# Kernel optimization log

Measured on AMD Instinct MI355X. Metric: run time of the kernel, lower is better.

The kernel has to match this reference:

```python
import jax, jax.numpy as jnp
import numpy as np

N, D, H = 262144, 512, 128


def _mlp(x, W1, b1, W2, b2):
    # Linear -> ReLU -> Linear
    return jax.nn.relu(x @ W1 + b1) @ W2 + b2


def setup_inputs() -> dict:
    key = jax.random.key(0)
    ks = jax.random.split(key, 8)
    features = jax.random.normal(ks[0], (N, D), dtype=jnp.float32)
    # last column is the routing flag: 0 -> transform expert, nonzero -> actor expert
    flags = jax.random.randint(ks[1], (N,), 0, 2).astype(jnp.float32)
    features = features.at[:, -1].set(flags)
    s = 0.02
    return {
        "features": features,
        "Wt1": jax.random.normal(ks[2], (D, H), dtype=jnp.float32) * s,
        "bt1": jnp.zeros((H,), dtype=jnp.float32),
        "Wt2": jax.random.normal(ks[3], (H, H), dtype=jnp.float32) * s,
        "bt2": jnp.zeros((H,), dtype=jnp.float32),
        "Wa1": jax.random.normal(ks[4], (D, H), dtype=jnp.float32) * s,
        "ba1": jnp.zeros((H,), dtype=jnp.float32),
        "Wa2": jax.random.normal(ks[5], (H, H), dtype=jnp.float32) * s,
        "ba2": jnp.zeros((H,), dtype=jnp.float32),
        "Wv1": jax.random.normal(ks[6], (D, H), dtype=jnp.float32) * s,
        "bv1": jnp.zeros((H,), dtype=jnp.float32),
        "Wv2": jax.random.normal(ks[7], (H, H), dtype=jnp.float32) * s,
        "bv2": jnp.zeros((H,), dtype=jnp.float32),
    }


def reference(features, Wt1, bt1, Wt2, bt2, Wa1, ba1, Wa2, ba2, Wv1, bv1, Wv2, bv2):
    # forward_actor: per-row dispatch on flag = features[:, -1]
    # flag == 0 -> policy_transform_net, else -> policy_actor_net.
    # Equivalent vectorized form: compute both experts, select per row.
    flag_is_zero = (features[:, -1] == 0)[:, None]  # [N, 1]
    trans_out = _mlp(features, Wt1, bt1, Wt2, bt2)   # [N, H]
    actor_out = _mlp(features, Wa1, ba1, Wa2, ba2)   # [N, H]
    latent_pi = jnp.where(flag_is_zero, trans_out, actor_out)
    # forward_critic: Linear-ReLU-Linear-ReLU
    latent_vf = jax.nn.relu(_mlp(features, Wv1, bv1, Wv2, bv2))
    return latent_pi, latent_vf
```

## Files before the change

kernel.cpp:

```cpp
#include <hip/hip_runtime.h>

#define NTOK 262144L

typedef __attribute__((ext_vector_type(4))) float f32x4;
typedef __attribute__((ext_vector_type(8))) short bf16x8;

static __device__ __forceinline__ unsigned short f2bf(float f) {
  unsigned int u = __builtin_bit_cast(unsigned int, f);
  u += 0x7fffu + ((u >> 16) & 1u);
  return (unsigned short)(u >> 16);
}

__global__ void pack_w(const float* __restrict__ Wt1, const float* __restrict__ Wa1,
                       const float* __restrict__ Wv1, const float* __restrict__ Wt2,
                       const float* __restrict__ Wa2, const float* __restrict__ Wv2,
                       unsigned short* __restrict__ pk) {
  int idx = blockIdx.x * 256 + threadIdx.x;
  if (idx >= 245760) return;
  float v;
  if (idx < 196608) {
    int j = idx & 7, l = (idx >> 3) & 63, ct = (idx >> 9) & 7, kt = (idx >> 12) & 15, e = idx >> 16;
    const float* W = (e == 0) ? Wt1 : (e == 1) ? Wa1 : Wv1;
    v = W[(kt * 32 + ((l >> 4) * 8) + j) * 128 + ct * 16 + (l & 15)];
  } else {
    int i2 = idx - 196608;
    int j = i2 & 7, l = (i2 >> 3) & 63, ct = (i2 >> 9) & 7, kt = (i2 >> 12) & 3, e = i2 >> 14;
    const float* W = (e == 0) ? Wt2 : (e == 1) ? Wa2 : Wv2;
    v = W[(kt * 32 + ((l >> 4) * 8) + j) * 128 + ct * 16 + (l & 15)];
  }
  pk[idx] = f2bf(v);
}


__global__ __launch_bounds__(512, 4) void mlp3(
    const float* __restrict__ X, const unsigned short* __restrict__ pk,
    const float* __restrict__ bt1, const float* __restrict__ bt2,
    const float* __restrict__ ba1, const float* __restrict__ ba2,
    const float* __restrict__ bv1, const float* __restrict__ bv2,
    float* __restrict__ out) {
  __shared__ unsigned short Xs[2 * 64 * 128];
  __shared__ unsigned short Hs[3 * 64 * 128];
  const int t = threadIdx.x;
  const long brow = (long)blockIdx.x * 64;
  const int lane = t & 63;
  const int w = t >> 6;
  const int l15 = lane & 15;
  const int g = lane >> 4;

  const float4* __restrict__ Xv = (const float4*)(X + brow * 512);

  f32x4 at[4], aa[4], av[4];
  {
    float b0 = bt1[w * 16 + l15], b1v = ba1[w * 16 + l15], b2v = bv1[w * 16 + l15];
    #pragma unroll
    for (int rt = 0; rt < 4; ++rt) {
      at[rt] = (f32x4){b0, b0, b0, b0};
      aa[rt] = (f32x4){b1v, b1v, b1v, b1v};
      av[rt] = (f32x4){b2v, b2v, b2v, b2v};
    }
  }

  {
    float4 ld[4];
    #pragma unroll
    for (int i = 0; i < 4; ++i) {
      int f = t + 512 * i;
      ld[i] = Xv[(f >> 5) * 128 + (f & 31)];
    }
    #pragma unroll
    for (int i = 0; i < 4; ++i) {
      int f = t + 512 * i;
      int row = f >> 5, c4 = f & 31;
      unsigned long long p = (unsigned long long)f2bf(ld[i].x)
                           | ((unsigned long long)f2bf(ld[i].y) << 16)
                           | ((unsigned long long)f2bf(ld[i].z) << 32)
                           | ((unsigned long long)f2bf(ld[i].w) << 48);
      int addr = (row * 256 + c4 * 8) ^ ((row & 7) << 4);
      *(unsigned long long*)((char*)Xs + addr) = p;
    }
  }
  __syncthreads();

  unsigned fmask = 0;

  #pragma unroll
  for (int kc = 0; kc < 4; ++kc) {
    float4 nx[4];
    if (kc < 3) {
      #pragma unroll
      for (int i = 0; i < 4; ++i) {
        int f = t + 512 * i;
        nx[i] = Xv[(f >> 5) * 128 + (kc + 1) * 32 + (f & 31)];
      }
    }
    const char* xb = (const char*)Xs + (kc & 1) * 16384;
    #pragma unroll
    for (int ktl = 0; ktl < 4; ++ktl) {
      int kt = kc * 4 + ktl;
      int wo = ((kt * 8 + w) << 9) + (lane << 3);
      bf16x8 wt = *(const bf16x8*)(pk + wo);
      bf16x8 wa = *(const bf16x8*)(pk + 65536 + wo);
      bf16x8 wv = *(const bf16x8*)(pk + 131072 + wo);
      #pragma unroll
      for (int rt = 0; rt < 4; ++rt) {
        int row = rt * 16 + l15;
        bf16x8 a = *(const bf16x8*)(xb + ((row * 256 + ktl * 64 + g * 16) ^ ((row & 7) << 4)));
        at[rt] = __builtin_amdgcn_mfma_f32_16x16x32_bf16(a, wt, at[rt], 0, 0, 0);
        aa[rt] = __builtin_amdgcn_mfma_f32_16x16x32_bf16(a, wa, aa[rt], 0, 0, 0);
        av[rt] = __builtin_amdgcn_mfma_f32_16x16x32_bf16(a, wv, av[rt], 0, 0, 0);
      }
    }
    if (kc == 3) {
      #pragma unroll
      for (int rt = 0; rt < 4; ++rt)
        #pragma unroll
        for (int r = 0; r < 4; ++r) {
          int row = rt * 16 + 4 * g + r;
          unsigned short fv = *(const unsigned short*)((const char*)Xs + 16384 +
                               ((row * 256 + 254) ^ ((row & 7) << 4)));
          if (fv != 0) fmask |= 1u << (rt * 4 + r);
        }
    }
    if (kc < 3) {
      #pragma unroll
      for (int i = 0; i < 4; ++i) {
        int f = t + 512 * i;
        int row = f >> 5, c4 = f & 31;
        unsigned long long p = (unsigned long long)f2bf(nx[i].x)
                             | ((unsigned long long)f2bf(nx[i].y) << 16)
                             | ((unsigned long long)f2bf(nx[i].z) << 32)
                             | ((unsigned long long)f2bf(nx[i].w) << 48);
        int addr = ((kc + 1) & 1) * 16384 + ((row * 256 + c4 * 8) ^ ((row & 7) << 4));
        *(unsigned long long*)((char*)Xs + addr) = p;
      }
      __syncthreads();
    }
  }

  #pragma unroll
  for (int rt = 0; rt < 4; ++rt)
    #pragma unroll
    for (int r = 0; r < 4; ++r) {
      int row = rt * 16 + 4 * g + r;
      int col = w * 16 + l15;
      int ha = (row * 256 + col * 2) ^ ((row & 7) << 4) ^ ((row & 8) << 2);
      *(unsigned short*)((char*)Hs + ha)         = f2bf(fmaxf(at[rt][r], 0.f));
      *(unsigned short*)((char*)Hs + 16384 + ha) = f2bf(fmaxf(aa[rt][r], 0.f));
      *(unsigned short*)((char*)Hs + 32768 + ha) = f2bf(fmaxf(av[rt][r], 0.f));
    }
  __syncthreads();

  auto layer2 = [&](int e, const float* __restrict__ b2, f32x4 a2[4]) {
    float bv = b2[w * 16 + l15];
    #pragma unroll
    for (int rt = 0; rt < 4; ++rt) a2[rt] = (f32x4){bv, bv, bv, bv};
    const unsigned short* W2f = pk + 196608 + e * 16384;
    const char* hb = (const char*)Hs + e * 16384;
    #pragma unroll
    for (int kt = 0; kt < 4; ++kt) {
      bf16x8 wb = *(const bf16x8*)(W2f + ((kt * 8 + w) << 9) + (lane << 3));
      #pragma unroll
      for (int rt = 0; rt < 4; ++rt) {
        int row = rt * 16 + l15;
        bf16x8 a = *(const bf16x8*)(hb + ((row * 256 + kt * 64 + g * 16)
                      ^ ((row & 7) << 4) ^ ((row & 8) << 2)));
        a2[rt] = __builtin_amdgcn_mfma_f32_16x16x32_bf16(a, wb, a2[rt], 0, 0, 0);
      }
    }
  };

  f32x4 keep[4], a2[4];
  layer2(0, bt2, keep);
  layer2(1, ba2, a2);
  {
    const int col = w * 16 + l15;
    #pragma unroll
    for (int rt = 0; rt < 4; ++rt)
      #pragma unroll
      for (int r = 0; r < 4; ++r) {
        long row = brow + rt * 16 + 4 * g + r;
        float sel = ((fmask >> (rt * 4 + r)) & 1u) ? a2[rt][r] : keep[rt][r];
        out[row * 128 + col] = sel;
      }
  }
  layer2(2, bv2, a2);
  {
    const int col = w * 16 + l15;
    float* __restrict__ ov = out + NTOK * 128;
    #pragma unroll
    for (int rt = 0; rt < 4; ++rt)
      #pragma unroll
      for (int r = 0; r < 4; ++r) {
        long row = brow + rt * 16 + 4 * g + r;
        ov[row * 128 + col] = fmaxf(a2[rt][r], 0.f);
      }
  }
}

extern "C" void kernel_launch(void* const* d_in, const int* in_sizes, int n_in,
                              void* d_out, int out_size, void* d_ws, size_t ws_size,
                              hipStream_t stream) {
  const float* X   = (const float*)d_in[0];
  const float* Wt1 = (const float*)d_in[1];
  const float* bt1 = (const float*)d_in[2];
  const float* Wt2 = (const float*)d_in[3];
  const float* bt2 = (const float*)d_in[4];
  const float* Wa1 = (const float*)d_in[5];
  const float* ba1 = (const float*)d_in[6];
  const float* Wa2 = (const float*)d_in[7];
  const float* ba2 = (const float*)d_in[8];
  const float* Wv1 = (const float*)d_in[9];
  const float* bv1 = (const float*)d_in[10];
  const float* Wv2 = (const float*)d_in[11];
  const float* bv2 = (const float*)d_in[12];
  unsigned short* pk = (unsigned short*)d_ws;

  pack_w<<<960, 256, 0, stream>>>(Wt1, Wa1, Wv1, Wt2, Wa2, Wv2, pk);
  mlp3<<<4096, 512, 0, stream>>>(X, pk, bt1, bt2, ba1, ba2, bv1, bv2, (float*)d_out);
}
```

Baseline: 271.7 us.

## Halve row tile to 32 with 4 waves each covering two column tiles

Each block now handles 32 rows with 256 threads, and each wave computes two 16-column tiles instead of one, so every A fragment read from LDS feeds twice as many MFMAs. Layer-2 hidden buffers shrink from three to two by reusing H0 for the critic branch, which adds extra barriers. LDS per block drops substantially, aiming for more resident blocks and better latency hiding. In exchange, each block does twice as many weight loads per row processed, and the grid doubles.

```diff
diff --git a/kernel.cpp b/kernel.cpp
--- a/kernel.cpp
+++ b/kernel.cpp
@@ -32,16 +32,17 @@
 }
 
 
-__global__ __launch_bounds__(512, 4) void mlp3(
+__global__ __launch_bounds__(256, 4) void mlp3(
     const float* __restrict__ X, const unsigned short* __restrict__ pk,
     const float* __restrict__ bt1, const float* __restrict__ bt2,
     const float* __restrict__ ba1, const float* __restrict__ ba2,
     const float* __restrict__ bv1, const float* __restrict__ bv2,
     float* __restrict__ out) {
-  __shared__ unsigned short Xs[2 * 64 * 128];
-  __shared__ unsigned short Hs[3 * 64 * 128];
+  __shared__ unsigned short Xs[2 * 32 * 128];
+  __shared__ unsigned short H0[32 * 128];
+  __shared__ unsigned short H1[32 * 128];
   const int t = threadIdx.x;
-  const long brow = (long)blockIdx.x * 64;
+  const long brow = (long)blockIdx.x * 32;
   const int lane = t & 63;
   const int w = t >> 6;
   const int l15 = lane & 15;
@@ -49,14 +50,17 @@
 
   const float4* __restrict__ Xv = (const float4*)(X + brow * 512);
 
-  f32x4 at[4], aa[4], av[4];
-  {
-    float b0 = bt1[w * 16 + l15], b1v = ba1[w * 16 + l15], b2v = bv1[w * 16 + l15];
-    #pragma unroll
-    for (int rt = 0; rt < 4; ++rt) {
-      at[rt] = (f32x4){b0, b0, b0, b0};
-      aa[rt] = (f32x4){b1v, b1v, b1v, b1v};
-      av[rt] = (f32x4){b2v, b2v, b2v, b2v};
+  f32x4 at[2][2], aa[2][2], av[2][2];
+  #pragma unroll
+  for (int c = 0; c < 2; ++c) {
+    float b0 = bt1[(2 * w + c) * 16 + l15];
+    float b1v = ba1[(2 * w + c) * 16 + l15];
+    float b2v = bv1[(2 * w + c) * 16 + l15];
+    #pragma unroll
+    for (int rt = 0; rt < 2; ++rt) {
+      at[rt][c] = (f32x4){b0, b0, b0, b0};
+      aa[rt][c] = (f32x4){b1v, b1v, b1v, b1v};
+      av[rt][c] = (f32x4){b2v, b2v, b2v, b2v};
     }
   }
 
@@ -64,12 +68,12 @@
     float4 ld[4];
     #pragma unroll
     for (int i = 0; i < 4; ++i) {
-      int f = t + 512 * i;
+      int f = t + 256 * i;
       ld[i] = Xv[(f >> 5) * 128 + (f & 31)];
     }
     #pragma unroll
     for (int i = 0; i < 4; ++i) {
-      int f = t + 512 * i;
+      int f = t + 256 * i;
       int row = f >> 5, c4 = f & 31;
       unsigned long long p = (unsigned long long)f2bf(ld[i].x)
                            | ((unsigned long long)f2bf(ld[i].y) << 16)
@@ -89,34 +93,40 @@
     if (kc < 3) {
       #pragma unroll
       for (int i = 0; i < 4; ++i) {
-        int f = t + 512 * i;
+        int f = t + 256 * i;
         nx[i] = Xv[(f >> 5) * 128 + (kc + 1) * 32 + (f & 31)];
       }
     }
-    const char* xb = (const char*)Xs + (kc & 1) * 16384;
+    const char* xb = (const char*)Xs + (kc & 1) * 8192;
     #pragma unroll
     for (int ktl = 0; ktl < 4; ++ktl) {
       int kt = kc * 4 + ktl;
-      int wo = ((kt * 8 + w) << 9) + (lane << 3);
-      bf16x8 wt = *(const bf16x8*)(pk + wo);
-      bf16x8 wa = *(const bf16x8*)(pk + 65536 + wo);
-      bf16x8 wv = *(const bf16x8*)(pk + 131072 + wo);
-      #pragma unroll
-      for (int rt = 0; rt < 4; ++rt) {
+      int wo0 = ((kt * 8 + 2 * w) << 9) + (lane << 3);
+      bf16x8 wt0 = *(const bf16x8*)(pk + wo0);
+      bf16x8 wt1v = *(const bf16x8*)(pk + wo0 + 512);
+      bf16x8 wa0 = *(const bf16x8*)(pk + 65536 + wo0);
+      bf16x8 wa1v = *(const bf16x8*)(pk + 65536 + wo0 + 512);
+      bf16x8 wv0 = *(const bf16x8*)(pk + 131072 + wo0);
+      bf16x8 wv1v = *(const bf16x8*)(pk + 131072 + wo0 + 512);
+      #pragma unroll
+      for (int rt = 0; rt < 2; ++rt) {
         int row = rt * 16 + l15;
         bf16x8 a = *(const bf16x8*)(xb + ((row * 256 + ktl * 64 + g * 16) ^ ((row & 7) << 4)));
-        at[rt] = __builtin_amdgcn_mfma_f32_16x16x32_bf16(a, wt, at[rt], 0, 0, 0);
-        aa[rt] = __builtin_amdgcn_mfma_f32_16x16x32_bf16(a, wa, aa[rt], 0, 0, 0);
-        av[rt] = __builtin_amdgcn_mfma_f32_16x16x32_bf16(a, wv, av[rt], 0, 0, 0);
+        at[rt][0] = __builtin_amdgcn_mfma_f32_16x16x32_bf16(a, wt0, at[rt][0], 0, 0, 0);
+        at[rt][1] = __builtin_amdgcn_mfma_f32_16x16x32_bf16(a, wt1v, at[rt][1], 0, 0, 0);
+        aa[rt][0] = __builtin_amdgcn_mfma_f32_16x16x32_bf16(a, wa0, aa[rt][0], 0, 0, 0);
+        aa[rt][1] = __builtin_amdgcn_mfma_f32_16x16x32_bf16(a, wa1v, aa[rt][1], 0, 0, 0);
+        av[rt][0] = __builtin_amdgcn_mfma_f32_16x16x32_bf16(a, wv0, av[rt][0], 0, 0, 0);
+        av[rt][1] = __builtin_amdgcn_mfma_f32_16x16x32_bf16(a, wv1v, av[rt][1], 0, 0, 0);
       }
     }
     if (kc == 3) {
       #pragma unroll
-      for (int rt = 0; rt < 4; ++rt)
+      for (int rt = 0; rt < 2; ++rt)
         #pragma unroll
         for (int r = 0; r < 4; ++r) {
           int row = rt * 16 + 4 * g + r;
-          unsigned short fv = *(const unsigned short*)((const char*)Xs + 16384 +
+          unsigned short fv = *(const unsigned short*)((const char*)Xs + 8192 +
                                ((row * 256 + 254) ^ ((row & 7) << 4)));
           if (fv != 0) fmask |= 1u << (rt * 4 + r);
         }
@@ -124,13 +134,13 @@
     if (kc < 3) {
       #pragma unroll
       for (int i = 0; i < 4; ++i) {
-        int f = t + 512 * i;
+        int f = t + 256 * i;
         int row = f >> 5, c4 = f & 31;
         unsigned long long p = (unsigned long long)f2bf(nx[i].x)
                              | ((unsigned long long)f2bf(nx[i].y) << 16)
                              | ((unsigned long long)f2bf(nx[i].z) << 32)
                              | ((unsigned long long)f2bf(nx[i].w) << 48);
-        int addr = ((kc + 1) & 1) * 16384 + ((row * 256 + c4 * 8) ^ ((row & 7) << 4));
+        int addr = (((kc + 1) & 1) * 8192) + ((row * 256 + c4 * 8) ^ ((row & 7) << 4));
         *(unsigned long long*)((char*)Xs + addr) = p;
       }
       __syncthreads();
@@ -138,63 +148,81 @@
   }
 
   #pragma unroll
-  for (int rt = 0; rt < 4; ++rt)
-    #pragma unroll
-    for (int r = 0; r < 4; ++r) {
-      int row = rt * 16 + 4 * g + r;
-      int col = w * 16 + l15;
-      int ha = (row * 256 + col * 2) ^ ((row & 7) << 4) ^ ((row & 8) << 2);
-      *(unsigned short*)((char*)Hs + ha)         = f2bf(fmaxf(at[rt][r], 0.f));
-      *(unsigned short*)((char*)Hs + 16384 + ha) = f2bf(fmaxf(aa[rt][r], 0.f));
-      *(unsigned short*)((char*)Hs + 32768 + ha) = f2bf(fmaxf(av[rt][r], 0.f));
-    }
-  __syncthreads();
-
-  auto layer2 = [&](int e, const float* __restrict__ b2, f32x4 a2[4]) {
-    float bv = b2[w * 16 + l15];
-    #pragma unroll
-    for (int rt = 0; rt < 4; ++rt) a2[rt] = (f32x4){bv, bv, bv, bv};
+  for (int rt = 0; rt < 2; ++rt)
+    #pragma unroll
+    for (int c = 0; c < 2; ++c)
+      #pragma unroll
+      for (int r = 0; r < 4; ++r) {
+        int row = rt * 16 + 4 * g + r;
+        int col = (2 * w + c) * 16 + l15;
+        int ha = (row * 256 + col * 2) ^ ((row & 7) << 4) ^ ((row & 8) << 2);
+        *(unsigned short*)((char*)H0 + ha) = f2bf(fmaxf(at[rt][c][r], 0.f));
+        *(unsigned short*)((char*)H1 + ha) = f2bf(fmaxf(aa[rt][c][r], 0.f));
+      }
+  __syncthreads();
+
+  auto layer2 = [&](const unsigned short* Hb, int e, const float* __restrict__ b2, f32x4 a2[2][2]) {
+    #pragma unroll
+    for (int c = 0; c < 2; ++c) {
+      float bv = b2[(2 * w + c) * 16 + l15];
+      a2[0][c] = (f32x4){bv, bv, bv, bv};
+      a2[1][c] = (f32x4){bv, bv, bv, bv};
+    }
     const unsigned short* W2f = pk + 196608 + e * 16384;
-    const char* hb = (const char*)Hs + e * 16384;
     #pragma unroll
     for (int kt = 0; kt < 4; ++kt) {
-      bf16x8 wb = *(const bf16x8*)(W2f + ((kt * 8 + w) << 9) + (lane << 3));
-      #pragma unroll
-      for (int rt = 0; rt < 4; ++rt) {
+      int wo = ((kt * 8 + 2 * w) << 9) + (lane << 3);
+      bf16x8 w0 = *(const bf16x8*)(W2f + wo);
+      bf16x8 w1 = *(const bf16x8*)(W2f + wo + 512);
+      #pragma unroll
+      for (int rt = 0; rt < 2; ++rt) {
         int row = rt * 16 + l15;
-        bf16x8 a = *(const bf16x8*)(hb + ((row * 256 + kt * 64 + g * 16)
-                      ^ ((row & 7) << 4) ^ ((row & 8) << 2)));
-        a2[rt] = __builtin_amdgcn_mfma_f32_16x16x32_bf16(a, wb, a2[rt], 0, 0, 0);
+        bf16x8 a = *(const bf16x8*)((const char*)Hb +
+                     ((row * 256 + kt * 64 + g * 16) ^ ((row & 7) << 4) ^ ((row & 8) << 2)));
+        a2[rt][0] = __builtin_amdgcn_mfma_f32_16x16x32_bf16(a, w0, a2[rt][0], 0, 0, 0);
+        a2[rt][1] = __builtin_amdgcn_mfma_f32_16x16x32_bf16(a, w1, a2[rt][1], 0, 0, 0);
       }
     }
   };
 
-  f32x4 keep[4], a2[4];
-  layer2(0, bt2, keep);
-  layer2(1, ba2, a2);
-  {
-    const int col = w * 16 + l15;
-    #pragma unroll
-    for (int rt = 0; rt < 4; ++rt)
+  f32x4 keep[2][2], a2[2][2];
+  layer2(H0, 0, bt2, keep);
+  layer2(H1, 1, ba2, a2);
+  #pragma unroll
+  for (int rt = 0; rt < 2; ++rt)
+    #pragma unroll
+    for (int c = 0; c < 2; ++c)
+      #pragma unroll
+      for (int r = 0; r < 4; ++r)
+        if ((fmask >> (rt * 4 + r)) & 1u) keep[rt][c][r] = a2[rt][c][r];
+  __syncthreads();
+
+  #pragma unroll
+  for (int rt = 0; rt < 2; ++rt)
+    #pragma unroll
+    for (int c = 0; c < 2; ++c)
+      #pragma unroll
+      for (int r = 0; r < 4; ++r) {
+        int row = rt * 16 + 4 * g + r;
+        int col = (2 * w + c) * 16 + l15;
+        int ha = (row * 256 + col * 2) ^ ((row & 7) << 4) ^ ((row & 8) << 2);
+        *(unsigned short*)((char*)H0 + ha) = f2bf(fmaxf(av[rt][c][r], 0.f));
+      }
+  __syncthreads();
+  layer2(H0, 2, bv2, a2);
+
+  float* __restrict__ ov = out + NTOK * 128;
+  #pragma unroll
+  for (int rt = 0; rt < 2; ++rt)
+    #pragma unroll
+    for (int c = 0; c < 2; ++c)
       #pragma unroll
       for (int r = 0; r < 4; ++r) {
         long row = brow + rt * 16 + 4 * g + r;
-        float sel = ((fmask >> (rt * 4 + r)) & 1u) ? a2[rt][r] : keep[rt][r];
-        out[row * 128 + col] = sel;
-      }
-  }
-  layer2(2, bv2, a2);
-  {
-    const int col = w * 16 + l15;
-    float* __restrict__ ov = out + NTOK * 128;
-    #pragma unroll
-    for (int rt = 0; rt < 4; ++rt)
-      #pragma unroll
-      for (int r = 0; r < 4; ++r) {
-        long row = brow + rt * 16 + 4 * g + r;
-        ov[row * 128 + col] = fmaxf(a2[rt][r], 0.f);
-      }
-  }
+        long col = (2 * w + c) * 16 + l15;
+        out[row * 128 + col] = keep[rt][c][r];
+        ov[row * 128 + col] = fmaxf(a2[rt][c][r], 0.f);
+      }
 }
 
 extern "C" void kernel_launch(void* const* d_in, const int* in_sizes, int n_in,
@@ -216,5 +244,5 @@
   unsigned short* pk = (unsigned short*)d_ws;
 
   pack_w<<<960, 256, 0, stream>>>(Wt1, Wa1, Wv1, Wt2, Wa2, Wv2, pk);
-  mlp3<<<4096, 512, 0, stream>>>(X, pk, bt1, bt2, ba1, ba2, bv1, bv2, (float*)d_out);
-}
+  mlp3<<<8192, 256, 0, stream>>>(X, pk, bt1, bt2, ba1, ba2, bv1, bv2, (float*)d_out);
+}
```

Measured after the change: 271.9 us. No clear change (+0.1%).
